# Kernel optimization log

Hardware: AMD Instinct MI355X
Metric: run time of the kernel (lower is better)

## Reference

```python
import jax, jax.numpy as jnp
import numpy as np

B, S, DM, H, DK, R, THETA = 8, 2048, 512, 8, 64, 128, 10000.0
BLK = R          # key/query block size; window radius == block size
NB = S // BLK    # number of blocks
NEG = -1e30      # additive mask for invalid positions (fp32-safe)


def setup_inputs() -> dict:
    key = jax.random.key(0)
    ks = jax.random.split(key, 5)
    scale = 0.02
    hidden_states = jax.random.normal(ks[0], (B, S, DM), jnp.float32)
    Wq = jax.random.normal(ks[1], (DM, H * DK), jnp.float32) * scale
    Wk = jax.random.normal(ks[2], (DM, H * DK), jnp.float32) * scale
    Wv = jax.random.normal(ks[3], (DM, H * DK), jnp.float32) * scale
    Wo = jax.random.normal(ks[4], (H * DK, DM), jnp.float32) * scale
    position_ids = jnp.tile(jnp.arange(S, dtype=jnp.int64)[None, :], (B, 1))
    return {"hidden_states": hidden_states, "Wq": Wq, "Wk": Wk, "Wv": Wv,
            "Wo": Wo, "position_ids": position_ids}


def _apply_rope(q, k, position_ids):
    # q,k: [B,H,S,DK]; position_ids: [B,S]
    half = DK // 2
    inv_freq = 1.0 / (THETA ** (jnp.arange(0, DK, 2, dtype=jnp.float32) / DK))  # [half]
    freqs = position_ids.astype(jnp.float32)[:, :, None] * inv_freq[None, None, :]  # [B,S,half]
    emb = jnp.concatenate([freqs, freqs], axis=-1)        # [B,S,DK]
    cos = jnp.cos(emb)[:, None, :, :]                     # [B,1,S,DK]
    sin = jnp.sin(emb)[:, None, :, :]

    def rotate_half(x):
        return jnp.concatenate([-x[..., half:], x[..., :half]], axis=-1)

    return q * cos + rotate_half(q) * sin, k * cos + rotate_half(k) * sin


def _band_mask():
    # valid[nb, BLK, 3*BLK]: key within [0,S) and |j - i| <= R
    b = jnp.arange(NB)[:, None, None]
    qi = jnp.arange(BLK)[None, :, None]
    kj = jnp.arange(3 * BLK)[None, None, :]
    kglob = (b - 1) * BLK + kj                 # global key index
    qglob = b * BLK + qi                        # global query index
    return (jnp.abs(kglob - qglob) <= R) & (kglob >= 0) & (kglob < S)


def reference(hidden_states, Wq, Wk, Wv, Wo, position_ids):
    # projections: [B,S,DM] -> [B,H,S,DK]
    def shape(x):
        return x.reshape(B, S, H, DK).transpose(0, 2, 1, 3)

    q = shape(hidden_states @ Wq)
    k = shape(hidden_states @ Wk)
    v = shape(hidden_states @ Wv)
    q, k = _apply_rope(q, k, position_ids)

    # block-banded sliding-window attention, softmax_scale = 1.0 (no scaling)
    pad = ((0, 0), (0, 0), (BLK, BLK), (0, 0))
    kb = jnp.pad(k, pad).reshape(B, H, NB + 2, BLK, DK)
    vb = jnp.pad(v, pad).reshape(B, H, NB + 2, BLK, DK)
    # neighbor window: blocks [b-1, b, b+1] -> [B,H,NB,3*BLK,DK]
    kwin = jnp.concatenate([kb[:, :, i:i + NB] for i in range(3)], axis=3)
    vwin = jnp.concatenate([vb[:, :, i:i + NB] for i in range(3)], axis=3)
    qb = q.reshape(B, H, NB, BLK, DK)

    scores = jnp.einsum('bhnqd,bhnkd->bhnqk', qb, kwin)   # unscaled
    valid = _band_mask()                                  # [NB,BLK,3*BLK]
    scores = jnp.where(valid[None, None], scores, NEG)
    attn = jax.nn.softmax(scores.astype(jnp.float32), axis=-1).astype(scores.dtype)
    outb = jnp.einsum('bhnqk,bhnkd->bhnqd', attn, vwin)   # [B,H,NB,BLK,DK]

    out = outb.reshape(B, H, S, DK).transpose(0, 2, 1, 3).reshape(B, S, H * DK)
    return out @ Wo
```

## Files before the change

### kernel.cpp

```cpp
#include <hip/hip_runtime.h>

using bf16 = __bf16;
typedef __bf16 bf16x8 __attribute__((ext_vector_type(8)));
typedef __bf16 bf16x4 __attribute__((ext_vector_type(4)));
typedef float f32x4 __attribute__((ext_vector_type(4)));
typedef float f32x16 __attribute__((ext_vector_type(16)));

#define MFMA16(a, b, c) __builtin_amdgcn_mfma_f32_16x16x32_bf16((a), (b), (c), 0, 0, 0)
#define MFMA32(a, b, c) __builtin_amdgcn_mfma_f32_32x32x16_bf16((a), (b), (c), 0, 0, 0)

constexpr int S = 2048, DM = 512, H = 8, DK = 64, HD = 512;
constexpr int NBLK = 16, BLK = 128;
constexpr int Mrows = 8 * S;
constexpr float LOG2E = 1.44269504088896340736f;

__device__ __forceinline__ void gll16(const void* g, void* l) {
  __builtin_amdgcn_global_load_lds((const __attribute__((address_space(1))) unsigned int*)g,
                                   (__attribute__((address_space(3))) unsigned int*)l, 16, 0, 0);
}

__global__ void k_prep(const float* __restrict__ hs,
                       const float* __restrict__ W0, const float* __restrict__ W1,
                       const float* __restrict__ W2, const float* __restrict__ W3,
                       bf16* __restrict__ Xb,
                       bf16* __restrict__ D0, bf16* __restrict__ D1,
                       bf16* __restrict__ D2, bf16* __restrict__ D3,
                       float2* __restrict__ ctab) {
  const int bid = blockIdx.x, t = threadIdx.x;
  __shared__ float tile[32][33];

  if (bid < 4096) {
    size_t i = ((size_t)bid * 256 + t) * 8;
    float4 a = *(const float4*)(hs + i);
    float4 b = *(const float4*)(hs + i + 4);
    bf16x8 o;
    o[0] = (bf16)a.x; o[1] = (bf16)a.y; o[2] = (bf16)a.z; o[3] = (bf16)a.w;
    o[4] = (bf16)b.x; o[5] = (bf16)b.y; o[6] = (bf16)b.z; o[7] = (bf16)b.w;
    *(bf16x8*)(Xb + i) = o;
    return;
  }
  if (bid < 5120) {
    const int b2 = bid - 4096;
    const int z = b2 >> 8, rem = b2 & 255;
    const int k0 = (rem & 15) * 32, n0 = (rem >> 4) * 32;
    const float* W = (z == 0) ? W0 : (z == 1) ? W1 : (z == 2) ? W2 : W3;
    bf16* Wt = (z == 0) ? D0 : (z == 1) ? D1 : (z == 2) ? D2 : D3;
    const int tx = t & 31, ty = t >> 5;
#pragma unroll
    for (int i = 0; i < 4; i++)
      tile[ty * 4 + i][tx] = W[(size_t)(k0 + ty * 4 + i) * 512 + n0 + tx];
    __syncthreads();
    if (z < 3) {
      if (t < 128) {
        int nin = t >> 2, cc = t & 3;
        bf16x8 o;
#pragma unroll
        for (int j = 0; j < 8; j++) o[j] = (bf16)tile[cc * 8 + j][nin];
        int n = n0 + nin;
        int ntile = n >> 4, ktile = k0 >> 5;
        int ll = (n & 15) + 16 * cc;
        *(bf16x8*)(Wt + ((size_t)(ntile * 16 + ktile)) * 512 + ll * 8) = o;
      }
    } else {
#pragma unroll
      for (int i = 0; i < 4; i++)
        Wt[(size_t)(n0 + ty * 4 + i) * 512 + k0 + tx] = (bf16)tile[tx][ty * 4 + i];
    }
    return;
  }
  {
    int idx = (bid - 5120) * 256 + t;
    int s = idx >> 5, i = idx & 31;
    float invf = exp2f(-(float)i * (13.287712379549449f / 32.0f));
    float ang = (float)s * invf;
    ctab[idx] = make_float2(cosf(ang), sinf(ang));
  }
}

__global__ __launch_bounds__(512) void k_gemm_qkv(
    const bf16* __restrict__ Xb,
    const bf16* __restrict__ Wfq, const bf16* __restrict__ Wfk, const bf16* __restrict__ Wfv,
    bf16* __restrict__ Qo, bf16* __restrict__ Ko, bf16* __restrict__ Vt,
    const float2* __restrict__ ctab) {
  const int bid = blockIdx.x;
  const int xcd = bid & 7, i = bid >> 3;
  const int mloc = i / 12, zy = i % 12;
  const int z = zy >> 2, y = zy & 3;
  const bf16* Wf = (z == 0) ? Wfq : ((z == 1) ? Wfk : Wfv);
  const float qscale = (z == 0) ? LOG2E : 1.0f;

  __shared__ __align__(16) char Asm3[3][16384];

  const int t = threadIdx.x, l = t & 63, wid = t >> 6;
  const int l15 = l & 15, l4 = l >> 4;
  const int wm = wid >> 1, wn = wid & 1;
  const size_t arow0 = (size_t)(xcd * 8 + mloc) * 256;
  const size_t brow0 = (size_t)y * 128;

  f32x4 acc[4][4] = {};
  const int rsb = wid * 16 + (l >> 2);
  const int cs = (l & 3) ^ ((l >> 3) & 3);

  const bf16* Bb = Wf + ((size_t)((int)(brow0 >> 4) + wn * 4)) * (16 * 512) + (size_t)l * 8;

  auto stage = [&](int kt, int b) {
    const int k0 = kt * 32;
    gll16(Xb + (arow0 + rsb) * 512 + k0 + cs * 8,       Asm3[b] + wid * 1024);
    gll16(Xb + (arow0 + 128 + rsb) * 512 + k0 + cs * 8, Asm3[b] + 8192 + wid * 1024);
  };

  stage(0, 0);
  stage(1, 1);
  asm volatile("s_waitcnt vmcnt(2)" ::: "memory");
  __builtin_amdgcn_s_barrier();

  int cur = 0;
  for (int kt = 0; kt < 16; ++kt) {
    if (kt + 2 <= 15) stage(kt + 2, (kt + 2) % 3);
    bf16x8 bfr[4];
#pragma unroll
    for (int ni = 0; ni < 4; ni++) bfr[ni] = *(const bf16x8*)(Bb + ni * 8192 + kt * 512);
    bf16x8 af[4];
#pragma unroll
    for (int mi = 0; mi < 4; mi++) {
      int row = wm * 64 + mi * 16 + l15;
      af[mi] = *(const bf16x8*)(Asm3[cur] + row * 64 + ((l4 ^ ((l15 >> 1) & 3)) * 16));
    }
#pragma unroll
    for (int mi = 0; mi < 4; mi++)
#pragma unroll
      for (int ni = 0; ni < 4; ni++)
        acc[mi][ni] = MFMA16(af[mi], bfr[ni], acc[mi][ni]);
    if (kt < 15) {
      if (kt < 14) asm volatile("s_waitcnt vmcnt(2)" ::: "memory");
      else         asm volatile("s_waitcnt vmcnt(0)" ::: "memory");
      __builtin_amdgcn_s_barrier();
    }
    cur = (cur == 2) ? 0 : cur + 1;
  }

  const int b = (int)(arow0 >> 11);
  const int hh = (int)(brow0 >> 6) + wn;

  if (z == 2) {
    const int sbase = (int)(arow0 & 2047) + wm * 64;
#pragma unroll
    for (int mi = 0; mi < 4; mi++) {
      int sg = (sbase + mi * 16) >> 4;
      int slo = l4 * 4;
#pragma unroll
      for (int ni = 0; ni < 4; ni++) {
        int dd = ni * 16 + l15;
        bf16x4 pk = {(bf16)acc[mi][ni][0], (bf16)acc[mi][ni][1],
                     (bf16)acc[mi][ni][2], (bf16)acc[mi][ni][3]};
        *(bf16x4*)(Vt + (((size_t)(b * H + hh) * 128 + sg) * 64 + dd) * 16 + slo) = pk;
      }
    }
    return;
  }

#pragma unroll
  for (int mi = 0; mi < 4; mi++) {
#pragma unroll
    for (int r = 0; r < 4; r++) {
      int grow = (int)arow0 + wm * 64 + mi * 16 + l4 * 4 + r;
      int s = grow & (S - 1);
      float2 cs0 = ctab[s * 32 + l15];
      float2 cs1 = ctab[s * 32 + 16 + l15];
#pragma unroll
      for (int ni = 0; ni < 4; ni++) {
        float a = acc[mi][ni][r];
        float b2 = acc[mi][ni ^ 2][r];
        float2 cc = (ni & 1) ? cs1 : cs0;
        float val = (ni < 2) ? (a * cc.x - b2 * cc.y) : (a * cc.x + b2 * cc.y);
        if (z == 0) {
          Qo[(size_t)grow * 512 + brow0 + wn * 64 + ni * 16 + l15] = (bf16)(val * qscale);
        } else {
          Ko[(((size_t)(b * H + hh) * 4 + ni) * 2048 + s) * 16 + l15] = (bf16)val;
        }
      }
    }
  }
}

__global__ __launch_bounds__(256) void k_gemm_out(
    const bf16* __restrict__ A, const bf16* __restrict__ Wt, float* __restrict__ out) {
  const int bid = blockIdx.x;
  const int xcd = bid & 7, i = bid >> 3;
  __shared__ __align__(16) char Asm3[3][8192];
  __shared__ __align__(16) char Bsm3[3][8192];

  const int t = threadIdx.x, l = t & 63, wid = t >> 6;
  const int l15 = l & 15, l4 = l >> 4;
  const int wm = wid >> 1, wn = wid & 1;
  const size_t arow0 = (size_t)(xcd * 16 + (i >> 2)) * 128;
  const size_t brow0 = (size_t)(i & 3) * 128;

  f32x4 acc[4][4] = {};
  const int rs = wid * 16 + (l >> 2);
  const int cs = (l & 3) ^ ((l >> 3) & 3);

  auto stage = [&](int kt, int b) {
    const int k0 = kt * 32;
    gll16(A + (arow0 + rs) * 512 + k0 + cs * 8,       Asm3[b] + wid * 1024);
    gll16(A + (arow0 + 64 + rs) * 512 + k0 + cs * 8,  Asm3[b] + 4096 + wid * 1024);
    gll16(Wt + (brow0 + rs) * 512 + k0 + cs * 8,      Bsm3[b] + wid * 1024);
    gll16(Wt + (brow0 + 64 + rs) * 512 + k0 + cs * 8, Bsm3[b] + 4096 + wid * 1024);
  };

  stage(0, 0);
  stage(1, 1);
  asm volatile("s_waitcnt vmcnt(4)" ::: "memory");
  __builtin_amdgcn_s_barrier();

  int cur = 0;
  for (int kt = 0; kt < 16; ++kt) {
    if (kt + 2 <= 15) stage(kt + 2, (kt + 2) % 3);
    bf16x8 af[4], bfr[4];
#pragma unroll
    for (int mi = 0; mi < 4; mi++) {
      int row = wm * 64 + mi * 16 + l15;
      af[mi] = *(const bf16x8*)(Asm3[cur] + row * 64 + ((l4 ^ ((l15 >> 1) & 3)) * 16));
    }
#pragma unroll
    for (int ni = 0; ni < 4; ni++) {
      int row = wn * 64 + ni * 16 + l15;
      bfr[ni] = *(const bf16x8*)(Bsm3[cur] + row * 64 + ((l4 ^ ((l15 >> 1) & 3)) * 16));
    }
#pragma unroll
    for (int mi = 0; mi < 4; mi++)
#pragma unroll
      for (int ni = 0; ni < 4; ni++)
        acc[mi][ni] = MFMA16(af[mi], bfr[ni], acc[mi][ni]);
    if (kt < 15) {
      if (kt < 14) asm volatile("s_waitcnt vmcnt(4)" ::: "memory");
      else         asm volatile("s_waitcnt vmcnt(0)" ::: "memory");
      __builtin_amdgcn_s_barrier();
    }
    cur = (cur == 2) ? 0 : cur + 1;
  }

#pragma unroll
  for (int mi = 0; mi < 4; mi++)
#pragma unroll
    for (int r = 0; r < 4; r++) {
      int grow = (int)arow0 + wm * 64 + mi * 16 + l4 * 4 + r;
      size_t rowoff = (size_t)grow * 512 + brow0 + wn * 64;
#pragma unroll
      for (int ni = 0; ni < 4; ni++)
        out[rowoff + ni * 16 + l15] = acc[mi][ni][r];
    }
}

__global__ __launch_bounds__(256, 4) void k_attn(
    const bf16* __restrict__ Q, const bf16* __restrict__ Kp, const bf16* __restrict__ VtP,
    bf16* __restrict__ O) {
  const int bid = blockIdx.x;
  const int swz = (bid & 7) * 128 + (bid >> 3);
  const int nb = swz & 15, h = (swz >> 4) & 7, bb = swz >> 7;
  const int t = threadIdx.x, l = t & 63, w = t >> 6;
  const int q31 = l & 31, hi = l >> 5;

  const int bh = bb * H + h;
  const size_t qrow = (size_t)bb * S + nb * BLK + w * 32 + q31;

  const bf16* Qp = Q + qrow * HD + h * DK + hi * 8;
  bf16x8 qb[4];
#pragma unroll
  for (int ks = 0; ks < 4; ks++) qb[ks] = *(const bf16x8*)(Qp + ks * 16);

  f32x16 o0 = {}, o1 = {};
  float mrun = -3e38f, lrun = 0.f;

  const bf16* Kbh = Kp + (size_t)bh * 131072;
  const bf16* Vbh = VtP + (size_t)bh * 131072;
  const int s0 = nb * BLK + w * 32 - 128;

  auto pv = [&](const f32x16& p, int kgc) {
    unsigned int Wd[4][2];
#pragma unroll
    for (int a = 0; a < 4; a++)
#pragma unroll
      for (int b2 = 0; b2 < 2; b2++) {
        unsigned int wd;
        asm("v_cvt_pk_bf16_f32 %0, %1, %2" : "=v"(wd) : "v"(p[4 * a + 2 * b2]), "v"(p[4 * a + 2 * b2 + 1]));
        Wd[a][b2] = wd;
      }
    bf16x8 pf[2];
#pragma unroll
    for (int ks = 0; ks < 2; ks++) {
      union { unsigned int u[4]; bf16x8 v; } cvt;
#pragma unroll
      for (int b2 = 0; b2 < 2; b2++) {
        unsigned int low_w = Wd[2 * ks][b2];
        unsigned int hi_w  = Wd[2 * ks + 1][b2];
        unsigned int msg = hi ? low_w : hi_w;
        unsigned int rec = __shfl_xor(msg, 32);
        cvt.u[b2]     = hi ? rec : low_w;
        cvt.u[2 + b2] = hi ? hi_w : rec;
      }
      pf[ks] = cvt.v;
    }
    const bf16* Vs = Vbh + (size_t)(kgc >> 4) * 1024 + q31 * 16 + hi * 8;
    __builtin_amdgcn_s_setprio(1);
    o0 = MFMA32(*(const bf16x8*)(Vs),               pf[0], o0);
    o0 = MFMA32(*(const bf16x8*)(Vs + 1024),        pf[1], o0);
    o1 = MFMA32(*(const bf16x8*)(Vs + 512),         pf[0], o1);
    o1 = MFMA32(*(const bf16x8*)(Vs + 1024 + 512),  pf[1], o1);
    __builtin_amdgcn_s_setprio(0);
  };

#pragma unroll
  for (int st = 0; st < 5; ++st) {
    const bool has2 = (st < 4);
    const int c0 = st * 2, c1 = c0 + 1;
    const int kg0 = s0 + c0 * 32, kg1 = s0 + c1 * 32;
    const int kc0 = kg0 < 0 ? 0 : (kg0 > S - 32 ? S - 32 : kg0);
    const int kc1 = kg1 < 0 ? 0 : (kg1 > S - 32 ? S - 32 : kg1);

    f32x16 a0 = {}, a1 = {};
    {
      const bf16* Kl = Kbh + (size_t)(kc0 + q31) * 16 + hi * 8;
      __builtin_amdgcn_s_setprio(1);
      a0 = MFMA32(*(const bf16x8*)(Kl),          qb[0], a0);
      a0 = MFMA32(*(const bf16x8*)(Kl + 32768),  qb[1], a0);
      a0 = MFMA32(*(const bf16x8*)(Kl + 65536),  qb[2], a0);
      a0 = MFMA32(*(const bf16x8*)(Kl + 98304),  qb[3], a0);
      __builtin_amdgcn_s_setprio(0);
    }
    if (has2) {
      const bf16* Kl = Kbh + (size_t)(kc1 + q31) * 16 + hi * 8;
      __builtin_amdgcn_s_setprio(1);
      a1 = MFMA32(*(const bf16x8*)(Kl),          qb[0], a1);
      a1 = MFMA32(*(const bf16x8*)(Kl + 32768),  qb[1], a1);
      a1 = MFMA32(*(const bf16x8*)(Kl + 65536),  qb[2], a1);
      a1 = MFMA32(*(const bf16x8*)(Kl + 98304),  qb[3], a1);
      __builtin_amdgcn_s_setprio(0);
    }

    if (kg0 != kc0) {
#pragma unroll
      for (int rg = 0; rg < 16; rg++) a0[rg] = -1e30f;
    } else if (c0 == 0) {
#pragma unroll
      for (int rg = 0; rg < 16; rg++) {
        int kk = (rg & 3) + 8 * (rg >> 2) + 4 * hi;
        if (kk < q31) a0[rg] = -1e30f;
      }
    } else if (c0 == 8) {
#pragma unroll
      for (int rg = 0; rg < 16; rg++) {
        int kk = (rg & 3) + 8 * (rg >> 2) + 4 * hi;
        if (kk > q31) a0[rg] = -1e30f;
      }
    }
    if (has2 && kg1 != kc1) {
#pragma unroll
      for (int rg = 0; rg < 16; rg++) a1[rg] = -1e30f;
    }

    f32x16 mx = a0;
    if (has2) {
#pragma unroll
      for (int rg = 0; rg < 16; rg++) mx[rg] = fmaxf(mx[rg], a1[rg]);
    }
#pragma unroll
    for (int sl = 8; sl >= 1; sl >>= 1)
#pragma unroll
      for (int i2 = 0; i2 < sl; i2++) mx[i2] = fmaxf(mx[i2], mx[i2 + sl]);
    const float pm = fmaxf(mx[0], __shfl_xor(mx[0], 32));

    if (!__all(pm - mrun <= 8.0f)) {
      const float mnew = fmaxf(mrun, pm);
      const float alpha = exp2f(mrun - mnew);
      lrun *= alpha;
#pragma unroll
      for (int rg = 0; rg < 16; rg++) { o0[rg] *= alpha; o1[rg] *= alpha; }
      mrun = mnew;
    }

    float rsum = 0.f;
#pragma unroll
    for (int rg = 0; rg < 16; rg++) { a0[rg] = exp2f(a0[rg] - mrun); rsum += a0[rg]; }
    if (has2) {
#pragma unroll
      for (int rg = 0; rg < 16; rg++) { a1[rg] = exp2f(a1[rg] - mrun); rsum += a1[rg]; }
    }
    rsum += __shfl_xor(rsum, 32);
    lrun += rsum;

    pv(a0, kc0);
    if (has2) pv(a1, kc1);
  }

  const float inv = 1.0f / lrun;
  bf16* Op = O + qrow * HD + h * DK + 4 * hi;
#pragma unroll
  for (int dt = 0; dt < 2; dt++) {
    const f32x16 oo = dt ? o1 : o0;
#pragma unroll
    for (int a = 0; a < 4; a++) {
      bf16x4 ob = {(bf16)(oo[4 * a + 0] * inv), (bf16)(oo[4 * a + 1] * inv),
                   (bf16)(oo[4 * a + 2] * inv), (bf16)(oo[4 * a + 3] * inv)};
      *(bf16x4*)(Op + dt * 32 + 8 * a) = ob;
    }
  }
}

extern "C" void kernel_launch(void* const* d_in, const int* in_sizes, int n_in,
                              void* d_out, int out_size, void* d_ws, size_t ws_size,
                              hipStream_t stream) {
  const float* hs = (const float*)d_in[0];
  const float* Wq = (const float*)d_in[1];
  const float* Wk = (const float*)d_in[2];
  const float* Wv = (const float*)d_in[3];
  const float* Wo = (const float*)d_in[4];
  float* out = (float*)d_out;

  char* ws = (char*)d_ws;
  const size_t MB = 1u << 20;
  bf16* Xb = (bf16*)(ws);
  bf16* Qb = (bf16*)(ws + 16 * MB);
  bf16* Kb = (bf16*)(ws + 32 * MB);
  bf16* Vt = (bf16*)(ws + 48 * MB);
  bf16* Wtq = (bf16*)(ws + 64 * MB);
  bf16* Wtk = Wtq + 512 * 512;
  bf16* Wtv = Wtk + 512 * 512;
  bf16* Wto = Wtv + 512 * 512;
  float2* ctab = (float2*)(ws + 64 * MB + 4 * 512 * 512 * sizeof(bf16));
  bf16* AO = Xb;

  k_prep<<<dim3(5376), dim3(256), 0, stream>>>(hs, Wq, Wk, Wv, Wo, Xb, Wtq, Wtk, Wtv, Wto, ctab);
  k_gemm_qkv<<<dim3(768), dim3(512), 0, stream>>>(Xb, Wtq, Wtk, Wtv, Qb, Kb, Vt, ctab);
  k_attn<<<dim3(NBLK * H * 8), dim3(256), 0, stream>>>(Qb, Kb, Vt, AO);
  k_gemm_out<<<dim3(512), dim3(256), 0, stream>>>(AO, Wto, out);
}
```

Before: 106.8 us.

## Use per-wave private LDS double buffers and register-prefetch B in QKV GEMM

The QKV projection GEMM replaces its shared triple-buffered A tile with a private double buffer per wave. Each wave stages only the 64 A rows it consumes, so the block-wide barriers in the k-loop go away. B fragments are now loaded one k-step ahead into registers and the loop is fully unrolled. In exchange, the two waves that share an M slice each load the same A rows, which doubles A global traffic. Prefetch depth also drops from two stages to one, and each step waits on vmcnt(0), so less load latency is hidden.

```diff
diff --git a/kernel.cpp b/kernel.cpp
--- a/kernel.cpp
+++ b/kernel.cpp
@@ -89,7 +89,7 @@
   const bf16* Wf = (z == 0) ? Wfq : ((z == 1) ? Wfk : Wfv);
   const float qscale = (z == 0) ? LOG2E : 1.0f;
 
-  __shared__ __align__(16) char Asm3[3][16384];
+  __shared__ __align__(16) char Asm[8][2][4096];
 
   const int t = threadIdx.x, l = t & 63, wid = t >> 6;
   const int l15 = l & 15, l4 = l >> 4;
@@ -98,45 +98,49 @@
   const size_t brow0 = (size_t)y * 128;
 
   f32x4 acc[4][4] = {};
-  const int rsb = wid * 16 + (l >> 2);
+  const int rlo = l >> 2;
   const int cs = (l & 3) ^ ((l >> 3) & 3);
+  char* myL = &Asm[wid][0][0];
 
   const bf16* Bb = Wf + ((size_t)((int)(brow0 >> 4) + wn * 4)) * (16 * 512) + (size_t)l * 8;
 
+  const bf16* Asrc = Xb + (arow0 + wm * 64 + rlo) * 512 + cs * 8;
+
   auto stage = [&](int kt, int b) {
-    const int k0 = kt * 32;
-    gll16(Xb + (arow0 + rsb) * 512 + k0 + cs * 8,       Asm3[b] + wid * 1024);
-    gll16(Xb + (arow0 + 128 + rsb) * 512 + k0 + cs * 8, Asm3[b] + 8192 + wid * 1024);
+    const bf16* src = Asrc + kt * 32;
+#pragma unroll
+    for (int j = 0; j < 4; j++)
+      gll16(src + (size_t)j * 16 * 512, myL + b * 4096 + j * 1024);
   };
 
   stage(0, 0);
-  stage(1, 1);
-  asm volatile("s_waitcnt vmcnt(2)" ::: "memory");
-  __builtin_amdgcn_s_barrier();
-
-  int cur = 0;
+  bf16x8 bcur[4];
+#pragma unroll
+  for (int ni = 0; ni < 4; ni++) bcur[ni] = *(const bf16x8*)(Bb + ni * 8192);
+
+#pragma unroll
   for (int kt = 0; kt < 16; ++kt) {
-    if (kt + 2 <= 15) stage(kt + 2, (kt + 2) % 3);
-    bf16x8 bfr[4];
-#pragma unroll
-    for (int ni = 0; ni < 4; ni++) bfr[ni] = *(const bf16x8*)(Bb + ni * 8192 + kt * 512);
+    asm volatile("s_waitcnt vmcnt(0)" ::: "memory");
     bf16x8 af[4];
 #pragma unroll
-    for (int mi = 0; mi < 4; mi++) {
-      int row = wm * 64 + mi * 16 + l15;
-      af[mi] = *(const bf16x8*)(Asm3[cur] + row * 64 + ((l4 ^ ((l15 >> 1) & 3)) * 16));
-    }
-#pragma unroll
     for (int mi = 0; mi < 4; mi++)
+      af[mi] = *(const bf16x8*)(myL + (kt & 1) * 4096 + (mi * 16 + l15) * 64 +
+                                ((l4 ^ ((l15 >> 1) & 3)) * 16));
+    if (kt < 15) stage(kt + 1, (kt + 1) & 1);
+    bf16x8 bnext[4];
+    if (kt < 15) {
+#pragma unroll
+      for (int ni = 0; ni < 4; ni++) bnext[ni] = *(const bf16x8*)(Bb + ni * 8192 + (kt + 1) * 512);
+    }
+#pragma unroll
+    for (int mi = 0; mi < 4; mi++)
 #pragma unroll
       for (int ni = 0; ni < 4; ni++)
-        acc[mi][ni] = MFMA16(af[mi], bfr[ni], acc[mi][ni]);
+        acc[mi][ni] = MFMA16(af[mi], bcur[ni], acc[mi][ni]);
     if (kt < 15) {
-      if (kt < 14) asm volatile("s_waitcnt vmcnt(2)" ::: "memory");
-      else         asm volatile("s_waitcnt vmcnt(0)" ::: "memory");
-      __builtin_amdgcn_s_barrier();
-    }
-    cur = (cur == 2) ? 0 : cur + 1;
+#pragma unroll
+      for (int ni = 0; ni < 4; ni++) bcur[ni] = bnext[ni];
+    }
   }
 
   const int b = (int)(arow0 >> 11);
```

New measurement: 120.4 us. 1.13x slower.
